# Performance work log

Hardware: AMD Instinct MI355X
Metric: run time of the kernel (lower is better)

Reference implementation:

```python
import jax, jax.numpy as jnp
import numpy as np
import math

H = 14
W = 14
MU_MAX = math.sqrt((H / 2) ** 2 + (W / 2) ** 2)
EPS = 1e-6
LN_EPS = 1e-5


def _distance_sq():
    fy = np.fft.fftfreq(H) * H
    fx = np.fft.rfftfreq(W) * W
    d = fy[:, None] ** 2 + fx[None, :] ** 2  # (H, W//2+1)
    return jnp.asarray(d[None, None], dtype=jnp.float32)  # (1,1,H,W//2+1)


def setup_inputs() -> dict:
    key = jax.random.key(0)
    k0, k1, k2 = jax.random.split(key, 3)
    B, C, HID = 256, 768, 192  # hidden = max(768//4, 8)
    return {
        "x": jax.random.normal(k0, (B, 197, C), jnp.float32),
        "ln_gamma": jnp.ones((C,), jnp.float32),
        "ln_beta": jnp.zeros((C,), jnp.float32),
        "w1": jax.random.normal(k1, (C, HID), jnp.float32) * 0.02,
        "b1": jnp.zeros((HID,), jnp.float32),
        "w2": jax.random.normal(k2, (HID, 2), jnp.float32) * 0.02,
        "b2": jnp.zeros((2,), jnp.float32),
        "residual_scale": jnp.asarray(1e-4, jnp.float32),
    }


def reference(x, ln_gamma, ln_beta, w1, b1, w2, b2, residual_scale):
    b, _, c = x.shape
    cls_tok = x[:, :1]          # (B,1,C)
    xs = x[:, 1:]               # (B,196,C) raw spatial tokens
    # LayerNorm (biased variance, eps=1e-5 like torch default)
    mu_ln = xs.mean(-1, keepdims=True)
    var_ln = xs.var(-1, keepdims=True)
    xn = (xs - mu_ln) / jnp.sqrt(var_ln + LN_EPS) * ln_gamma + ln_beta
    # to (B,C,H,W) grid
    xg = xn.transpose(0, 2, 1).reshape(b, c, H, W)
    xm = xg.mean((-2, -1), keepdims=True)
    spec = jnp.fft.rfft2(xg - xm, norm='ortho')  # (B,C,H,W//2+1) complex
    energy = jnp.log1p(jnp.abs(spec)).mean((-2, -1))  # (B,C)
    hdn = jax.nn.gelu(energy @ w1 + b1, approximate=False)
    out2 = hdn @ w2 + b2  # (B,2)
    mu = jnp.maximum(MU_MAX * jax.nn.sigmoid(out2[:, 0]), 1.0).reshape(b, 1, 1, 1)
    sigma = jnp.maximum(jax.nn.softplus(out2[:, 1]), 0.1).reshape(b, 1, 1, 1)
    mask = jnp.exp(-_distance_sq() / (2.0 * mu ** 2 * sigma + EPS))
    filtered = jnp.fft.irfft2(spec * mask, s=(H, W), norm='ortho') + xm
    toks = filtered.reshape(b, c, H * W).transpose(0, 2, 1)  # (B,196,C)
    delta = toks - xn
    return jnp.concatenate([cls_tok, xs + residual_scale * delta], axis=1)
```

## Files before the change

kernel.cpp:

```cpp
#include <hip/hip_runtime.h>
#include <hip/hip_fp16.h>
#include <math.h>

#define NB    256
#define NTOKP 197
#define NTOK  196
#define NC    768
#define NHID  192
#define NH    14
#define NVF   8
#define CHT   64
#define NTILE 12

constexpr float CT14[14] = {
    1.0f, 0.9009688679024191f, 0.6234898018587336f, 0.22252093395631445f,
    -0.22252093395631434f, -0.6234898018587335f, -0.9009688679024191f, -1.0f,
    -0.9009688679024191f, -0.6234898018587335f, -0.22252093395631434f,
    0.22252093395631445f, 0.6234898018587336f, 0.9009688679024191f};
constexpr float ST14[14] = {
    0.0f, 0.4338837391175581f, 0.7818314824680298f, 0.9749279121818236f,
    0.9749279121818236f, 0.7818314824680299f, 0.43388373911755823f, 0.0f,
    -0.43388373911755823f, -0.7818314824680299f, -0.9749279121818236f,
    -0.9749279121818236f, -0.7818314824680298f, -0.4338837391175581f};

__device__ __forceinline__ unsigned int h2bits(__half2 h) {
  return *(unsigned int*)&h;
}

template <bool WH>
__global__ __launch_bounds__(256) void k_stats(const float* __restrict__ x,
                                               const float* __restrict__ gamma,
                                               const float* __restrict__ beta,
                                               float2* __restrict__ msv,
                                               __half* __restrict__ xnh) {
  int row = blockIdx.x * 4 + (threadIdx.x >> 6);
  int lane = threadIdx.x & 63;
  if (row >= NB * NTOK) return;
  int b = row / NTOK, t = row - b * NTOK;
  const float4* p = (const float4*)(x + ((size_t)b * NTOKP + 1 + t) * NC);
  float4 v[3];
  float s = 0.f, ss = 0.f;
#pragma unroll
  for (int k = 0; k < 3; ++k) {
    v[k] = p[lane + k * 64];
    s += v[k].x + v[k].y + v[k].z + v[k].w;
    ss += v[k].x * v[k].x + v[k].y * v[k].y + v[k].z * v[k].z + v[k].w * v[k].w;
  }
#pragma unroll
  for (int m = 32; m; m >>= 1) {
    s += __shfl_xor(s, m);
    ss += __shfl_xor(ss, m);
  }
  float mean = s * (1.f / NC);
  float var = ss * (1.f / NC) - mean * mean;
  float rstd = rsqrtf(var + 1e-5f);
  if (lane == 0) msv[row] = make_float2(mean, rstd);
  if (WH) {
#pragma unroll
    for (int k = 0; k < 3; ++k) {
      float4 g = ((const float4*)gamma)[lane + k * 64];
      float4 be = ((const float4*)beta)[lane + k * 64];
      float4 xn;
      xn.x = (v[k].x - mean) * rstd * g.x + be.x;
      xn.y = (v[k].y - mean) * rstd * g.y + be.y;
      xn.z = (v[k].z - mean) * rstd * g.z + be.z;
      xn.w = (v[k].w - mean) * rstd * g.w + be.w;
      uint2 u = make_uint2(h2bits(__floats2half2_rn(xn.x, xn.y)),
                           h2bits(__floats2half2_rn(xn.z, xn.w)));
      *(uint2*)(xnh + (size_t)row * NC + lane * 4 + k * 256) = u;
    }
  }
}

template <bool UH>
__global__ __launch_bounds__(256) void k_fwd(const float* __restrict__ x,
                                             const __half* __restrict__ xnh,
                                             const float* __restrict__ gamma,
                                             const float* __restrict__ beta,
                                             const float2* __restrict__ msv,
                                             const float* __restrict__ w1,
                                             __half* __restrict__ partial) {
  __shared__ __half2 A[NH * NVF * CHT];
  __shared__ float2 ms[UH ? 1 : NTOK];
  __shared__ float esum[256];
  __shared__ float el[CHT];
  int b = blockIdx.y, c0 = blockIdx.x * CHT, tid = threadIdx.x;
  int c = tid & 63, w = tid >> 6;

  float g = 0.f, be = 0.f;
  if (!UH) {
    for (int k = tid; k < NTOK; k += 256) ms[k] = msv[b * NTOK + k];
    g = gamma[c0 + c];
    be = beta[c0 + c];
  }

  __half2 TW1[14], TW2[14];
#pragma unroll
  for (int k = 0; k < 14; ++k) {
    TW1[k] = __floats2half2_rn(CT14[k], -ST14[k]);
    TW2[k] = __floats2half2_rn(ST14[k], CT14[k]);
  }
  __syncthreads();

#pragma unroll 1
  for (int i = w; i < NH; i += 4) {
    __half2 xh[NH];
    if (UH) {
      const __half* xr = xnh + ((size_t)b * NTOK + i * NH) * NC + c0 + c;
#pragma unroll
      for (int j = 0; j < NH; ++j) xh[j] = __half2half2(xr[(size_t)j * NC]);
    } else {
      const float* xr = x + ((size_t)b * NTOKP + 1 + i * NH) * NC + c0 + c;
#pragma unroll
      for (int j = 0; j < NH; ++j) {
        float2 m = ms[i * NH + j];
        xh[j] = __float2half2_rn((xr[(size_t)j * NC] - m.x) * m.y * g + be);
      }
    }
    __half2 acc[NVF];
#pragma unroll
    for (int v = 0; v < NVF; ++v) acc[v] = __floats2half2_rn(0.f, 0.f);
#pragma unroll
    for (int j = 0; j < NH; ++j) {
#pragma unroll
      for (int v = 0; v < NVF; ++v)
        acc[v] = __hfma2(xh[j], TW1[(v * j) % 14], acc[v]);
    }
#pragma unroll
    for (int v = 0; v < NVF; ++v) A[(i * NVF + v) * CHT + c] = acc[v];
  }
  __syncthreads();

  float part = 0.f;
#pragma unroll 1
  for (int vv = 0; vv < 2; ++vv) {
    int v = w * 2 + vv;
    bool herm = (v == 0) || (v == 7);
    const __half2* Ac = A + v * CHT + c;
    __half2 E[7], O[7];
#pragma unroll
    for (int k = 0; k < 7; ++k) {
      E[k] = __floats2half2_rn(0.f, 0.f);
      O[k] = __floats2half2_rn(0.f, 0.f);
    }
#pragma unroll
    for (int m = 0; m < 7; ++m) {
      __half2 ae = Ac[(2 * m) * NVF * CHT];
      __half2 ao = Ac[(2 * m + 1) * NVF * CHT];
      __half2 aer = __low2half2(ae), aei = __high2half2(ae);
      __half2 aor = __low2half2(ao), aoi = __high2half2(ao);
#pragma unroll
      for (int k = 0; k < 7; ++k) {
        int t = (2 * k * m) % 14;
        E[k] = __hfma2(aer, TW1[t], __hfma2(aei, TW2[t], E[k]));
        O[k] = __hfma2(aor, TW1[t], __hfma2(aoi, TW2[t], O[k]));
      }
    }
    float pa = 1.f, pb = 1.f;
#pragma unroll
    for (int u = 0; u < 14; ++u) {
      if (!herm || u < 8) {
        int k = u % 7;
        __half2 Ov = O[k];
        __half2 S = __hfma2(__low2half2(Ov), TW1[u],
                            __hfma2(__high2half2(Ov), TW2[u], E[k]));
        float2 s2 = __half22float2(S);
        float mag = 14.f + __builtin_amdgcn_sqrtf(fmaf(s2.x, s2.x, s2.y * s2.y));
        if (herm) {
          float msq = mag * mag;
          if (u == 0) {
            if (v == 7) pb *= mag;
          } else if (u <= 3) {
            pa *= msq;
          } else if (u <= 6) {
            pb *= msq;
          } else {
            pb *= mag;
          }
        } else {
          if (u < 7) pa *= mag; else pb *= mag;
        }
      }
    }
    part += __logf(pa) + __logf(pb);
  }
  esum[tid] = part;
  __syncthreads();
  if (w == 0) {
    float e = esum[c] + esum[c + 64] + esum[c + 128] + esum[c + 192];
    el[c] = (e - 111.f * 2.6390573296152584f) * (1.f / 112.f);
  }
  __syncthreads();
  if (tid < NHID) {
    float acc = 0.f;
#pragma unroll 8
    for (int cc = 0; cc < CHT; ++cc)
      acc = fmaf(el[cc], w1[(size_t)(c0 + cc) * NHID + tid], acc);
    partial[((size_t)b * NTILE + blockIdx.x) * NHID + tid] = __float2half(acc);
  }
}

template <bool UH>
__global__ __launch_bounds__(256) void k_inv(const float* __restrict__ x,
                                             const __half* __restrict__ xnh,
                                             const float* __restrict__ gamma,
                                             const float* __restrict__ beta,
                                             const float2* __restrict__ msv,
                                             const __half* __restrict__ partial,
                                             const float* __restrict__ b1,
                                             const float* __restrict__ w2,
                                             const float* __restrict__ b2,
                                             const float* __restrict__ rscale,
                                             float* __restrict__ out) {
  __shared__ __half2 T[NH * 7 * CHT];
  __shared__ float2 ms[NTOK];
  __shared__ float rr[UH ? NTOK : 1];
  __shared__ float wexp[NH];
  __shared__ float kc[NH];
  __shared__ float2 sh2[NHID];
  __shared__ float msb_sh;
  int b = blockIdx.y, c0 = blockIdx.x * CHT, tid = threadIdx.x;
  int c = tid & 63, w = tid >> 6;
  float rs = rscale[0];

  for (int k = tid; k < NTOK; k += 256) {
    float2 m = msv[b * NTOK + k];
    ms[k] = m;
    if (UH) rr[k] = 1.f / m.y;
  }
  if (tid < CHT) {
    size_t idx = (size_t)b * NTOKP * NC + c0 + tid;
    out[idx] = x[idx];
  }
  if (tid < NHID) {
    float a = b1[tid];
#pragma unroll
    for (int s = 0; s < NTILE; ++s)
      a += __half2float(partial[((size_t)b * NTILE + s) * NHID + tid]);
    float ge = 0.5f * a * (1.f + erff(a * 0.70710678118654752f));
    sh2[tid] = make_float2(ge * w2[2 * tid], ge * w2[2 * tid + 1]);
  }
  __syncthreads();
  if (tid < 64) {
    float p0 = sh2[tid].x + sh2[tid + 64].x + sh2[tid + 128].x;
    float p1 = sh2[tid].y + sh2[tid + 64].y + sh2[tid + 128].y;
#pragma unroll
    for (int off = 32; off; off >>= 1) {
      p0 += __shfl_down(p0, off);
      p1 += __shfl_down(p1, off);
    }
    if (tid == 0) {
      float o0 = p0 + b2[0], o1 = p1 + b2[1];
      float muv = fmaxf(9.899494936611665f / (1.f + expf(-o0)), 1.f);
      float sp = (o1 > 20.f) ? o1 : log1pf(expf(o1));
      float sg = fmaxf(sp, 0.1f);
      msb_sh = 2.f * muv * muv * sg + 1e-6f;
    }
  }
  __syncthreads();
  float msb = msb_sh;
  if (tid < NH) {
    int f = (tid <= 7) ? tid : 14 - tid;
    wexp[tid] = __expf(-(float)(f * f) / msb);
  }
  __syncthreads();
  if (tid < NH) {
    float s = 0.f;
#pragma unroll
    for (int k = 0; k < NH; ++k) s = fmaf(wexp[k], CT14[(k * tid) % 14], s);
    kc[tid] = s * (1.f / 14.f);
  }
  float g = gamma[c0 + c], be = beta[c0 + c];
  float rg = 1.f / g;
  __syncthreads();

  float kr[NH];
#pragma unroll
  for (int d = 0; d < NH; ++d) kr[d] = kc[d];
  __half2 khp[NH];
#pragma unroll
  for (int d = 0; d < NH; ++d) khp[d] = __floats2half2_rn(kr[d], kr[(d + 1) % 14]);

#pragma unroll 1
  for (int i = w; i < NH; i += 4) {
    __half2 xh[NH];
    if (UH) {
      const __half* xr = xnh + ((size_t)b * NTOK + i * NH) * NC + c0 + c;
#pragma unroll
      for (int j = 0; j < NH; ++j) xh[j] = __half2half2(xr[(size_t)j * NC]);
    } else {
      const float* xr = x + ((size_t)b * NTOKP + 1 + i * NH) * NC + c0 + c;
#pragma unroll
      for (int j = 0; j < NH; ++j) {
        float2 m = ms[i * NH + j];
        xh[j] = __float2half2_rn((xr[(size_t)j * NC] - m.x) * m.y * g + be);
      }
    }
#pragma unroll
    for (int jp = 0; jp < 7; ++jp) {
      __half2 acc = __floats2half2_rn(0.f, 0.f);
#pragma unroll
      for (int j = 0; j < NH; ++j)
        acc = __hfma2(xh[j], khp[(2 * jp - j + 28) % 14], acc);
      T[(i * 7 + jp) * CHT + c] = acc;
    }
  }
  __syncthreads();

#pragma unroll 1
  for (int jq = w; jq < NH; jq += 4) {
    int jp = jq >> 1, hi = jq & 1;
    __half2 acc2[7];
#pragma unroll
    for (int d = 0; d < 7; ++d) acc2[d] = __floats2half2_rn(0.f, 0.f);
#pragma unroll
    for (int i = 0; i < NH; ++i) {
      __half2 t = T[(i * 7 + jp) * CHT + c];
      __half2 yi = hi ? __high2half2(t) : __low2half2(t);
#pragma unroll
      for (int d = 0; d < 7; ++d)
        acc2[d] = __hfma2(yi, khp[(2 * d - i + 28) % 14], acc2[d]);
    }
    float* outr = out + ((size_t)b * NTOKP + 1 + jq) * NC + c0 + c;
    const __half* xq = xnh + ((size_t)b * NTOK + jq) * NC + c0 + c;
    const float* xr = x + ((size_t)b * NTOKP + 1 + jq) * NC + c0 + c;
#pragma unroll
    for (int ii = 0; ii < NH; ++ii) {
      float z = (ii & 1) ? __high2float(acc2[ii >> 1]) : __low2float(acc2[ii >> 1]);
      if (UH) {
        float xnv = __half2float(xq[(size_t)ii * NH * NC]);
        int t = ii * NH + jq;
        float xv = fmaf((xnv - be) * rg, rr[t], ms[t].x);
        outr[(size_t)ii * NH * NC] = xv + rs * (z - xnv);
      } else {
        float xv = xr[(size_t)ii * NH * NC];
        float2 m = ms[ii * NH + jq];
        float xn = (xv - m.x) * m.y * g + be;
        outr[(size_t)ii * NH * NC] = xv + rs * (z - xn);
      }
    }
  }
}

extern "C" void kernel_launch(void* const* d_in, const int* in_sizes, int n_in,
                              void* d_out, int out_size, void* d_ws, size_t ws_size,
                              hipStream_t stream) {
  (void)in_sizes; (void)n_in; (void)out_size;
  const float* x      = (const float*)d_in[0];
  const float* gamma  = (const float*)d_in[1];
  const float* beta   = (const float*)d_in[2];
  const float* w1     = (const float*)d_in[3];
  const float* b1     = (const float*)d_in[4];
  const float* w2     = (const float*)d_in[5];
  const float* b2     = (const float*)d_in[6];
  const float* rscale = (const float*)d_in[7];
  float* out = (float*)d_out;

  char* wsb = (char*)d_ws;
  float2* msv     = (float2*)(wsb + 0);
  __half* partial = (__half*)(wsb + 401408);
  __half* xnh     = (__half*)(wsb + 1581056);
  size_t need = 1581056 + (size_t)NB * NTOK * NC * 2;
  bool useH = ws_size >= need;

  if (useH) {
    k_stats<true><<<NB * NTOK / 4, 256, 0, stream>>>(x, gamma, beta, msv, xnh);
    k_fwd<true><<<dim3(NTILE, NB), 256, 0, stream>>>(x, xnh, gamma, beta, msv,
                                                     w1, partial);
    k_inv<true><<<dim3(NTILE, NB), 256, 0, stream>>>(x, xnh, gamma, beta, msv,
                                                     partial, b1, w2, b2,
                                                     rscale, out);
  } else {
    k_stats<false><<<NB * NTOK / 4, 256, 0, stream>>>(x, gamma, beta, msv, xnh);
    k_fwd<false><<<dim3(NTILE, NB), 256, 0, stream>>>(x, xnh, gamma, beta, msv,
                                                      w1, partial);
    k_inv<false><<<dim3(NTILE, NB), 256, 0, stream>>>(x, xnh, gamma, beta, msv,
                                                      partial, b1, w2, b2,
                                                      rscale, out);
  }
}
```

Measured before the change: 137.1 us.

## Use MFMA matrix ops for the separable 2D circular filter in inverse kernel

Adds a new inverse kernel that stages the fp16 normalized tokens in LDS and applies the 14x14 circulant filter as two 16x16x16 MFMA products (rows then columns), padding to 16. The filtered values are written to an LDS buffer and then combined with the residual in a coalesced token-major pass. This replaces per-thread packed-half FMA convolution loops with matrix-core work, at the cost of more LDS usage (which may reduce occupancy) and fp16 rounding of the intermediate result. The fallback path is simplified to the fp32-only variant.

```diff
diff --git a/kernel.cpp b/kernel.cpp
--- a/kernel.cpp
+++ b/kernel.cpp
@@ -11,6 +11,11 @@
 #define NVF   8
 #define CHT   64
 #define NTILE 12
+#define XSTR  268
+#define ZSTR  66
+
+typedef _Float16 f16x4 __attribute__((ext_vector_type(4)));
+typedef float f32x4 __attribute__((ext_vector_type(4)));
 
 constexpr float CT14[14] = {
     1.0f, 0.9009688679024191f, 0.6234898018587336f, 0.22252093395631445f,
@@ -200,9 +205,142 @@
   }
 }
 
-template <bool UH>
+__global__ __launch_bounds__(256) void k_inv_mf(const float* __restrict__ x,
+                                                const __half* __restrict__ xnh_,
+                                                const float* __restrict__ gamma,
+                                                const float* __restrict__ beta,
+                                                const float2* __restrict__ msv,
+                                                const __half* __restrict__ partial,
+                                                const float* __restrict__ b1,
+                                                const float* __restrict__ w2,
+                                                const float* __restrict__ b2,
+                                                const float* __restrict__ rscale,
+                                                float* __restrict__ out) {
+  __shared__ _Float16 Xl[CHT * XSTR];
+  __shared__ _Float16 Zl[NTOK * ZSTR];
+  __shared__ _Float16 Kf[16 * 16];
+  __shared__ float2 ms[NTOK];
+  __shared__ float rr[NTOK];
+  __shared__ float wexp[NH];
+  __shared__ float kc[NH];
+  __shared__ float2 sh2[NHID];
+  __shared__ float msb_sh;
+  int b = blockIdx.y, c0 = blockIdx.x * CHT, tid = threadIdx.x;
+  int l = tid & 63, w = tid >> 6;
+  const _Float16* xnh = (const _Float16*)xnh_;
+  float rs = rscale[0];
+
+  for (int k = tid; k < NTOK; k += 256) {
+    float2 m = msv[b * NTOK + k];
+    ms[k] = m;
+    rr[k] = 1.f / m.y;
+  }
+  if (tid < CHT) {
+    size_t idx = (size_t)b * NTOKP * NC + c0 + tid;
+    out[idx] = x[idx];
+  }
+  if (tid < NHID) {
+    float a = b1[tid];
+#pragma unroll
+    for (int s = 0; s < NTILE; ++s)
+      a += __half2float(partial[((size_t)b * NTILE + s) * NHID + tid]);
+    float ge = 0.5f * a * (1.f + erff(a * 0.70710678118654752f));
+    sh2[tid] = make_float2(ge * w2[2 * tid], ge * w2[2 * tid + 1]);
+  }
+  __syncthreads();
+  if (tid < 64) {
+    float p0 = sh2[tid].x + sh2[tid + 64].x + sh2[tid + 128].x;
+    float p1 = sh2[tid].y + sh2[tid + 64].y + sh2[tid + 128].y;
+#pragma unroll
+    for (int off = 32; off; off >>= 1) {
+      p0 += __shfl_down(p0, off);
+      p1 += __shfl_down(p1, off);
+    }
+    if (tid == 0) {
+      float o0 = p0 + b2[0], o1 = p1 + b2[1];
+      float muv = fmaxf(9.899494936611665f / (1.f + expf(-o0)), 1.f);
+      float sp = (o1 > 20.f) ? o1 : log1pf(expf(o1));
+      float sg = fmaxf(sp, 0.1f);
+      msb_sh = 2.f * muv * muv * sg + 1e-6f;
+    }
+  }
+  __syncthreads();
+  if (tid < NH) {
+    int f = (tid <= 7) ? tid : 14 - tid;
+    wexp[tid] = __expf(-(float)(tid <= 7 ? f * f : f * f) / msb_sh);
+  }
+  __syncthreads();
+  if (tid < NH) {
+    float s = 0.f;
+#pragma unroll
+    for (int k = 0; k < NH; ++k) s = fmaf(wexp[k], CT14[(k * tid) % 14], s);
+    kc[tid] = s * (1.f / 14.f);
+  }
+  __syncthreads();
+  {
+    int a = tid >> 4, bb2 = tid & 15;
+    Kf[tid] = (a < 14 && bb2 < 14) ? (_Float16)kc[(a - bb2 + 14) % 14]
+                                   : (_Float16)0.f;
+  }
+#pragma unroll 1
+  for (int i = w; i < NH; i += 4) {
+    const _Float16* xr = xnh + ((size_t)b * NTOK + i * NH) * NC + c0 + l;
+#pragma unroll
+    for (int jg = 0; jg < 4; ++jg) {
+      f16x4 hv;
+#pragma unroll
+      for (int e = 0; e < 4; ++e) {
+        int j = jg * 4 + e;
+        hv[e] = (j < NH) ? xr[(size_t)j * NC] : (_Float16)0.f;
+      }
+      *(f16x4*)&Xl[l * XSTR + i * 16 + jg * 4] = hv;
+    }
+  }
+  if (tid < 128) {
+    int ch = tid & 63, r = 14 + (tid >> 6);
+    f16x4 z4 = {(_Float16)0.f, (_Float16)0.f, (_Float16)0.f, (_Float16)0.f};
+#pragma unroll
+    for (int jg = 0; jg < 4; ++jg) *(f16x4*)&Xl[ch * XSTR + r * 16 + jg * 4] = z4;
+  }
+  __syncthreads();
+
+  f16x4 kb;
+#pragma unroll
+  for (int q = 0; q < 4; ++q) kb[q] = Kf[((l >> 4) * 4 + q) * 16 + (l & 15)];
+  f32x4 zero4 = {0.f, 0.f, 0.f, 0.f};
+
+#pragma unroll 1
+  for (int cc = 0; cc < 16; ++cc) {
+    int ch = w * 16 + cc;
+    f16x4 xa = *(const f16x4*)&Xl[ch * XSTR + (l & 15) * 16 + (l >> 4) * 4];
+    f32x4 y = __builtin_amdgcn_mfma_f32_16x16x16f16(xa, kb, zero4, 0, 0, 0);
+    f16x4 yh;
+#pragma unroll
+    for (int q = 0; q < 4; ++q) yh[q] = (_Float16)y[q];
+    f32x4 z = __builtin_amdgcn_mfma_f32_16x16x16f16(kb, yh, zero4, 0, 0, 0);
+    int jp = l & 15;
+    if (jp < NH) {
+#pragma unroll
+      for (int q = 0; q < 4; ++q) {
+        int ii = (l >> 4) * 4 + q;
+        if (ii < NH) Zl[(ii * NH + jp) * ZSTR + ch] = (_Float16)z[q];
+      }
+    }
+  }
+  __syncthreads();
+
+  float g = gamma[c0 + l], be = beta[c0 + l];
+  float rg = 1.f / g;
+#pragma unroll 1
+  for (int t = w; t < NTOK; t += 4) {
+    float z = (float)Zl[t * ZSTR + l];
+    float xnv = (float)xnh[((size_t)b * NTOK + t) * NC + c0 + l];
+    float xv = fmaf((xnv - be) * rg, rr[t], ms[t].x);
+    out[((size_t)b * NTOKP + 1 + t) * NC + c0 + l] = xv + rs * (z - xnv);
+  }
+}
+
 __global__ __launch_bounds__(256) void k_inv(const float* __restrict__ x,
-                                             const __half* __restrict__ xnh,
                                              const float* __restrict__ gamma,
                                              const float* __restrict__ beta,
                                              const float2* __restrict__ msv,
@@ -214,7 +352,6 @@
                                              float* __restrict__ out) {
   __shared__ __half2 T[NH * 7 * CHT];
   __shared__ float2 ms[NTOK];
-  __shared__ float rr[UH ? NTOK : 1];
   __shared__ float wexp[NH];
   __shared__ float kc[NH];
   __shared__ float2 sh2[NHID];
@@ -223,11 +360,7 @@
   int c = tid & 63, w = tid >> 6;
   float rs = rscale[0];
 
-  for (int k = tid; k < NTOK; k += 256) {
-    float2 m = msv[b * NTOK + k];
-    ms[k] = m;
-    if (UH) rr[k] = 1.f / m.y;
-  }
+  for (int k = tid; k < NTOK; k += 256) ms[k] = msv[b * NTOK + k];
   if (tid < CHT) {
     size_t idx = (size_t)b * NTOKP * NC + c0 + tid;
     out[idx] = x[idx];
@@ -271,7 +404,6 @@
     kc[tid] = s * (1.f / 14.f);
   }
   float g = gamma[c0 + c], be = beta[c0 + c];
-  float rg = 1.f / g;
   __syncthreads();
 
   float kr[NH];
@@ -283,18 +415,12 @@
 
 #pragma unroll 1
   for (int i = w; i < NH; i += 4) {
+    const float* xr = x + ((size_t)b * NTOKP + 1 + i * NH) * NC + c0 + c;
     __half2 xh[NH];
-    if (UH) {
-      const __half* xr = xnh + ((size_t)b * NTOK + i * NH) * NC + c0 + c;
-#pragma unroll
-      for (int j = 0; j < NH; ++j) xh[j] = __half2half2(xr[(size_t)j * NC]);
-    } else {
-      const float* xr = x + ((size_t)b * NTOKP + 1 + i * NH) * NC + c0 + c;
-#pragma unroll
-      for (int j = 0; j < NH; ++j) {
-        float2 m = ms[i * NH + j];
-        xh[j] = __float2half2_rn((xr[(size_t)j * NC] - m.x) * m.y * g + be);
-      }
+#pragma unroll
+    for (int j = 0; j < NH; ++j) {
+      float2 m = ms[i * NH + j];
+      xh[j] = __float2half2_rn((xr[(size_t)j * NC] - m.x) * m.y * g + be);
     }
 #pragma unroll
     for (int jp = 0; jp < 7; ++jp) {
@@ -322,22 +448,14 @@
         acc2[d] = __hfma2(yi, khp[(2 * d - i + 28) % 14], acc2[d]);
     }
     float* outr = out + ((size_t)b * NTOKP + 1 + jq) * NC + c0 + c;
-    const __half* xq = xnh + ((size_t)b * NTOK + jq) * NC + c0 + c;
     const float* xr = x + ((size_t)b * NTOKP + 1 + jq) * NC + c0 + c;
 #pragma unroll
     for (int ii = 0; ii < NH; ++ii) {
       float z = (ii & 1) ? __high2float(acc2[ii >> 1]) : __low2float(acc2[ii >> 1]);
-      if (UH) {
-        float xnv = __half2float(xq[(size_t)ii * NH * NC]);
-        int t = ii * NH + jq;
-        float xv = fmaf((xnv - be) * rg, rr[t], ms[t].x);
-        outr[(size_t)ii * NH * NC] = xv + rs * (z - xnv);
-      } else {
-        float xv = xr[(size_t)ii * NH * NC];
-        float2 m = ms[ii * NH + jq];
-        float xn = (xv - m.x) * m.y * g + be;
-        outr[(size_t)ii * NH * NC] = xv + rs * (z - xn);
-      }
+      float xv = xr[(size_t)ii * NH * NC];
+      float2 m = ms[ii * NH + jq];
+      float xn = (xv - m.x) * m.y * g + be;
+      outr[(size_t)ii * NH * NC] = xv + rs * (z - xn);
     }
   }
 }
@@ -367,15 +485,14 @@
     k_stats<true><<<NB * NTOK / 4, 256, 0, stream>>>(x, gamma, beta, msv, xnh);
     k_fwd<true><<<dim3(NTILE, NB), 256, 0, stream>>>(x, xnh, gamma, beta, msv,
                                                      w1, partial);
-    k_inv<true><<<dim3(NTILE, NB), 256, 0, stream>>>(x, xnh, gamma, beta, msv,
-                                                     partial, b1, w2, b2,
-                                                     rscale, out);
+    k_inv_mf<<<dim3(NTILE, NB), 256, 0, stream>>>(x, xnh, gamma, beta, msv,
+                                                  partial, b1, w2, b2, rscale,
+                                                  out);
   } else {
     k_stats<false><<<NB * NTOK / 4, 256, 0, stream>>>(x, gamma, beta, msv, xnh);
     k_fwd<false><<<dim3(NTILE, NB), 256, 0, stream>>>(x, xnh, gamma, beta, msv,
                                                       w1, partial);
-    k_inv<false><<<dim3(NTILE, NB), 256, 0, stream>>>(x, xnh, gamma, beta, msv,
-                                                      partial, b1, w2, b2,
-                                                      rscale, out);
-  }
-}
+    k_inv<<<dim3(NTILE, NB), 256, 0, stream>>>(x, gamma, beta, msv, partial,
+                                               b1, w2, b2, rscale, out);
+  }
+}
```

After: 173.4 us. +26.5%, slower.
